# Kernel optimization log

Measured on AMD Instinct MI355X. Metric: run time of the kernel, lower is better.

The kernel has to match this reference:

```python
import jax, jax.numpy as jnp
import numpy as np

EMBED_DIM = 1024
NUM_HEADS = 16
HEAD_DIM = EMBED_DIM // NUM_HEADS
FF_HIDDEN = 4096
ROPE_BASE = 10000.0


def rope(x, start_pos):
    # x: [B, H, S, hd]; interleaved pair rotation
    S, hd = x.shape[2], x.shape[3]
    freqs = 1.0 / ROPE_BASE ** (jnp.arange(0, hd, 2, dtype=jnp.float32) / hd)
    t = jnp.arange(start_pos, start_pos + S, dtype=jnp.float32)
    angles = jnp.outer(t, freqs)            # [S, hd/2]
    cos, sin = jnp.cos(angles), jnp.sin(angles)
    x_even = x[..., 0::2]
    x_odd = x[..., 1::2]
    out_even = x_even * cos - x_odd * sin
    out_odd = x_even * sin + x_odd * cos
    return jnp.stack((out_even, out_odd), axis=-1).reshape(x.shape)


def rmsnorm(x, w, eps=1e-6):
    rms = jnp.sqrt(jnp.mean(x * x, axis=-1, keepdims=True) + eps)
    return x / rms * w


def setup_inputs() -> dict:
    key = jax.random.key(0)
    ks = jax.random.split(key, 8)
    D, H = EMBED_DIM, FF_HIDDEN
    s = lambda fin: 1.0 / np.sqrt(fin)
    return {
        "x": jax.random.normal(ks[0], (2, 2048, D), dtype=jnp.float32),
        "start_pos": 0,
        "norm1_w": jnp.ones((D,), jnp.float32),
        "w_qkv": jax.random.uniform(ks[1], (3 * D, D), jnp.float32, -s(D), s(D)),
        "w_o": jax.random.uniform(ks[2], (D, D), jnp.float32, -s(D), s(D)),
        "norm2_w": jnp.ones((D,), jnp.float32),
        "w_gate": jax.random.uniform(ks[3], (H, D), jnp.float32, -s(D), s(D)),
        "w_up": jax.random.uniform(ks[4], (H, D), jnp.float32, -s(D), s(D)),
        "w_down": jax.random.uniform(ks[5], (D, H), jnp.float32, -s(H), s(H)),
    }


def attention(x, w_qkv, w_o, start_pos):
    B, S, D = x.shape
    qkv = x @ w_qkv.T                         # [B, S, 3D]
    q, k, v = jnp.split(qkv, 3, axis=-1)
    def heads(t):
        return t.reshape(B, S, NUM_HEADS, HEAD_DIM).transpose(0, 2, 1, 3)
    q, k, v = heads(q), heads(k), heads(v)    # [B, H, S, hd]
    q = rope(q, start_pos)
    k = rope(k, start_pos)
    scores = jnp.einsum('bhqd,bhkd->bhqk', q, k) / np.sqrt(HEAD_DIM)
    causal = jnp.tril(jnp.ones((S, S), dtype=bool))
    scores = jnp.where(causal, scores, -jnp.inf)
    attn = jax.nn.softmax(scores, axis=-1)
    out = jnp.einsum('bhqk,bhkd->bhqd', attn, v)
    out = out.transpose(0, 2, 1, 3).reshape(B, S, D)
    return out @ w_o.T


def ffn(x, w_gate, w_up, w_down):
    return (jax.nn.silu(x @ w_gate.T) * (x @ w_up.T)) @ w_down.T


def reference(x, start_pos, norm1_w, w_qkv, w_o, norm2_w, w_gate, w_up, w_down):
    x = x + attention(rmsnorm(x, norm1_w), w_qkv, w_o, start_pos)
    x = x + ffn(rmsnorm(x, norm2_w), w_gate, w_up, w_down)
    return x
```

## Files before the change

### kernel.cpp

```cpp
#include <hip/hip_runtime.h>
#include <math.h>

typedef __bf16 bf16_t;
typedef __bf16 bf16x2 __attribute__((ext_vector_type(2)));
typedef __bf16 bf16x4 __attribute__((ext_vector_type(4)));
typedef __bf16 bf16x8 __attribute__((ext_vector_type(8)));
typedef float f32x4 __attribute__((ext_vector_type(4)));

#define B_ 2
#define S_ 2048
#define D_ 1024
#define NH 16
#define HD 64
#define FF 4096
#define NTOK (B_*S_)

__device__ __forceinline__ f32x4 mfma16(bf16x8 a, bf16x8 b, f32x4 c) {
  return __builtin_amdgcn_mfma_f32_16x16x32_bf16(a, b, c, 0, 0, 0);
}

__device__ __forceinline__ void gld_lds16(const bf16_t* g, bf16_t* l) {
  __builtin_amdgcn_global_load_lds(
      (const __attribute__((address_space(1))) void*)g,
      (__attribute__((address_space(3))) void*)l, 16, 0, 0);
}

__global__ __launch_bounds__(256) void cvt5_kernel(
    const float* __restrict__ p0, const float* __restrict__ p1,
    const float* __restrict__ p2, const float* __restrict__ p3,
    const float* __restrict__ p4,
    bf16_t* __restrict__ o0, bf16_t* __restrict__ o1, bf16_t* __restrict__ o2,
    bf16_t* __restrict__ o3, bf16_t* __restrict__ o4) {
  int i = blockIdx.x * 256 + threadIdx.x;
  const int stride = gridDim.x * 256;
  const int n = 4194304;
  for (; i < n; i += stride) {
    const float* src; bf16_t* dst; int j = i;
    if (j < 786432) { src = p0; dst = o0; }
    else {
      j -= 786432;
      if (j < 262144) { src = p1; dst = o1; }
      else {
        j -= 262144;
        if (j < 1048576) { src = p2; dst = o2; }
        else {
          j -= 1048576;
          if (j < 1048576) { src = p3; dst = o3; }
          else { j -= 1048576; src = p4; dst = o4; }
        }
      }
    }
    float4 v = ((const float4*)src)[j];
    bf16x4 ov;
    ov[0] = (bf16_t)v.x; ov[1] = (bf16_t)v.y; ov[2] = (bf16_t)v.z; ov[3] = (bf16_t)v.w;
    ((bf16x4*)dst)[j] = ov;
  }
}

__global__ __launch_bounds__(256) void rmsnorm_kernel(const float* __restrict__ x,
                                                      const float* __restrict__ w,
                                                      bf16_t* __restrict__ o) {
  const int row = blockIdx.x;
  const float4 v = ((const float4*)(x + (size_t)row * D_))[threadIdx.x];
  float s = v.x*v.x + v.y*v.y + v.z*v.z + v.w*v.w;
  #pragma unroll
  for (int d = 32; d; d >>= 1) s += __shfl_down(s, d);
  __shared__ float acc[4];
  if ((threadIdx.x & 63) == 0) acc[threadIdx.x >> 6] = s;
  __syncthreads();
  const float scale = rsqrtf((acc[0] + acc[1] + acc[2] + acc[3]) * (1.f / D_) + 1e-6f);
  const float4 wv = ((const float4*)w)[threadIdx.x];
  bf16x4 ov;
  ov[0] = (bf16_t)(v.x * scale * wv.x);
  ov[1] = (bf16_t)(v.y * scale * wv.y);
  ov[2] = (bf16_t)(v.z * scale * wv.z);
  ov[3] = (bf16_t)(v.w * scale * wv.w);
  ((bf16x4*)(o + (size_t)row * D_))[threadIdx.x] = ov;
}

template<int MODE, int BN>
__global__ __launch_bounds__(256) void gemm_kernel(
    const bf16_t* __restrict__ A, const bf16_t* __restrict__ W,
    int M, int N, int K,
    float* __restrict__ outF, bf16_t* __restrict__ outB,
    const float* __restrict__ res, const bf16_t* __restrict__ gate) {
  constexpr int NB = BN / 32;
  __shared__ __align__(16) bf16_t lA[2][128 * 32];
  __shared__ __align__(16) bf16_t lB[2][BN * 32];
  const int tid = threadIdx.x;
  const int wave = tid >> 6, lane = tid & 63;
  const int r = lane & 15, kg = lane >> 4;
  const int bm = blockIdx.y * 128, bn = blockIdx.x * BN;
  const int wr = (wave >> 1) * 64, wc = (wave & 1) * (BN / 2);
  const bf16_t* Ab = A + (size_t)bm * K;
  const bf16_t* Wb = W + (size_t)bn * K;

  auto stage = [&](int buf, int k0) {
    const int cb0 = (wave << 6);
    const int c0 = cb0 + lane;
    gld_lds16(Ab + (size_t)(c0 >> 2) * K + k0 + (c0 & 3) * 8, lA[buf] + cb0 * 8);
    const int cb1 = cb0 + 256;
    const int c1 = cb1 + lane;
    gld_lds16(Ab + (size_t)(c1 >> 2) * K + k0 + (c1 & 3) * 8, lA[buf] + cb1 * 8);
    gld_lds16(Wb + (size_t)(c0 >> 2) * K + k0 + (c0 & 3) * 8, lB[buf] + cb0 * 8);
    if (BN == 128)
      gld_lds16(Wb + (size_t)(c1 >> 2) * K + k0 + (c1 & 3) * 8, lB[buf] + cb1 * 8);
  };

  f32x4 acc[4][NB] = {};
  stage(0, 0);
  asm volatile("s_waitcnt vmcnt(0)" ::: "memory");
  __syncthreads();
  int cur = 0;
  for (int k0 = 0; k0 < K; k0 += 32) {
    if (k0 + 32 < K) stage(cur ^ 1, k0 + 32);
    const bf16_t* cA = lA[cur];
    const bf16_t* cB = lB[cur];
    bf16x8 af[4], bfr[NB];
    #pragma unroll
    for (int m = 0; m < 4; ++m)
      af[m] = *(const bf16x8*)&cA[(wr + m * 16 + r) * 32 + kg * 8];
    #pragma unroll
    for (int n = 0; n < NB; ++n)
      bfr[n] = *(const bf16x8*)&cB[(wc + n * 16 + r) * 32 + kg * 8];
    #pragma unroll
    for (int m = 0; m < 4; ++m)
      #pragma unroll
      for (int n = 0; n < NB; ++n)
        acc[m][n] = mfma16(af[m], bfr[n], acc[m][n]);
    asm volatile("s_waitcnt vmcnt(0)" ::: "memory");
    __syncthreads();
    cur ^= 1;
  }
  #pragma unroll
  for (int m = 0; m < 4; ++m) {
    const int row0 = bm + wr + m * 16 + kg * 4;
    #pragma unroll
    for (int n = 0; n < NB; ++n) {
      const int col = bn + wc + n * 16 + r;
      #pragma unroll
      for (int g2 = 0; g2 < 4; ++g2) {
        const size_t idx = (size_t)(row0 + g2) * N + col;
        const float v = acc[m][n][g2];
        if (MODE == 0) {
          outB[idx] = (bf16_t)v;
        } else if (MODE == 1) {
          outF[idx] = v + res[idx];
        } else {
          const float gf = (float)gate[idx];
          outB[idx] = (bf16_t)(v * gf / (1.f + __expf(-gf)));
        }
      }
    }
  }
}

__global__ __launch_bounds__(256) void rope_kernel(const bf16_t* __restrict__ qkv,
                                                   bf16_t* __restrict__ q_r,
                                                   bf16_t* __restrict__ k_r,
                                                   const int* __restrict__ start_pos) {
  const int bs = blockIdx.x;
  const int b = bs >> 11, s = bs & (S_ - 1);
  const float t = (float)(s + start_pos[0]);
  const bf16_t* rowp = qkv + (size_t)bs * 3072;
  #pragma unroll
  for (int i = 0; i < 4; ++i) {
    const int p = threadIdx.x + 256 * i;
    const int mat = p >> 9;
    const int rem = p & 511;
    const int h = rem >> 5, d2 = rem & 31;
    const float freq = exp2f((float)d2 * -0.4152410118609203f);
    float sn, cs;
    sincosf(t * freq, &sn, &cs);
    const float qs = mat ? 1.0f : 0.18033688011112042f;
    const bf16x2 e2 = *(const bf16x2*)(rowp + mat * 1024 + h * 64 + 2 * d2);
    const float e = (float)e2[0], od = (float)e2[1];
    bf16x2 ov;
    ov[0] = (bf16_t)((e * cs - od * sn) * qs);
    ov[1] = (bf16_t)((e * sn + od * cs) * qs);
    bf16_t* dst = (mat ? k_r : q_r) + ((size_t)(b * NH + h) * S_ + s) * HD + 2 * d2;
    *(bf16x2*)dst = ov;
  }
}

__global__ __launch_bounds__(256) void vtrans_kernel(const bf16_t* __restrict__ qkv,
                                                     bf16_t* __restrict__ vt) {
  const int bh = blockIdx.y, b = bh >> 4, h = bh & 15;
  const int s0 = blockIdx.x * 64;
  __shared__ bf16_t tile[64][65];
  #pragma unroll
  for (int i = 0; i < 16; ++i) {
    const int idx = threadIdx.x + 256 * i;
    const int sl = idx >> 6, d = idx & 63;
    tile[sl][d] = qkv[(size_t)(b * S_ + s0 + sl) * 3072 + 2048 + h * 64 + d];
  }
  __syncthreads();
  #pragma unroll
  for (int i = 0; i < 16; ++i) {
    const int idx = threadIdx.x + 256 * i;
    const int dl = idx >> 6, sl = idx & 63;
    vt[((size_t)bh * HD + dl) * S_ + s0 + sl] = tile[sl][dl];
  }
}

__global__ __launch_bounds__(256, 4) void attn_kernel(const bf16_t* __restrict__ qr,
                                                      const bf16_t* __restrict__ kr,
                                                      const bf16_t* __restrict__ vt,
                                                      bf16_t* __restrict__ out) {
  const int lid = blockIdx.x + 32 * blockIdx.y;
  const int xcd = lid & 7, slot = lid >> 3;
  const int bh = xcd * 4 + (slot >> 5);
  const int bx = slot & 31;
  const int b = bh >> 4, h = bh & 15;
  const int wave = threadIdx.x >> 6, lane = threadIdx.x & 63;
  const int pl = wave >> 1, sub = wave & 1;
  const int r = lane & 15, kg = lane >> 4;
  const int pairIdx = bx * 2 + pl;
  const bf16_t* kb_p = kr + (size_t)bh * S_ * HD;
  const bf16_t* vb_p = vt + (size_t)bh * HD * S_;

  __shared__ __align__(16) f32x4 lo[2][4][64];
  __shared__ float lm[2][64], ll[2][64];

  auto kv_block = [&](int kb, int qbase, const bf16x8& qf0, const bf16x8& qf1,
                      f32x4* o, float& m, float& l, bool masked) {
    f32x4 st[4];
    #pragma unroll
    for (int f = 0; f < 4; ++f) {
      const bf16_t* kp = kb_p + (size_t)(kb + f * 16 + r) * HD;
      f32x4 z = {};
      z = mfma16(*(const bf16x8*)&kp[kg * 8], qf0, z);
      z = mfma16(*(const bf16x8*)&kp[32 + kg * 8], qf1, z);
      st[f] = z;
    }
    float sc[4][4];
    float mx = -1e30f;
    #pragma unroll
    for (int f = 0; f < 4; ++f)
      #pragma unroll
      for (int g2 = 0; g2 < 4; ++g2) {
        float v = st[f][g2];
        if (masked) {
          const int k = kb + f * 16 + kg * 4 + g2;
          v = (k <= qbase + r) ? v : -1e30f;
        }
        sc[f][g2] = v;
        mx = fmaxf(mx, v);
      }
    mx = fmaxf(mx, __shfl_xor(mx, 16));
    mx = fmaxf(mx, __shfl_xor(mx, 32));
    float alpha = 1.f;
    const bool need = !__all(mx - m <= 8.f);
    if (need) {
      const float nm = fmaxf(m, mx);
      alpha = exp2f(m - nm);
      m = nm;
    }
    float psum = 0.f;
    float pe[4][4];
    #pragma unroll
    for (int f = 0; f < 4; ++f)
      #pragma unroll
      for (int g2 = 0; g2 < 4; ++g2) {
        const float p = exp2f(sc[f][g2] - m);
        pe[f][g2] = p;
        psum += p;
      }
    psum += __shfl_xor(psum, 16);
    psum += __shfl_xor(psum, 32);
    l = l * alpha + psum;
    bf16x8 PA[2];
    #pragma unroll
    for (int fa = 0; fa < 2; ++fa) {
      bf16x8 v;
      #pragma unroll
      for (int j = 0; j < 4; ++j) v[j] = (bf16_t)pe[2 * fa][j];
      #pragma unroll
      for (int j = 0; j < 4; ++j) v[4 + j] = (bf16_t)pe[2 * fa + 1][j];
      PA[fa] = v;
    }
    if (need) {
      float av[4];
      #pragma unroll
      for (int g2 = 0; g2 < 4; ++g2) av[g2] = __shfl(alpha, kg * 4 + g2);
      #pragma unroll
      for (int dblk = 0; dblk < 4; ++dblk)
        #pragma unroll
        for (int g2 = 0; g2 < 4; ++g2) o[dblk][g2] *= av[g2];
    }
    #pragma unroll
    for (int dblk = 0; dblk < 4; ++dblk) {
      const bf16_t* vp = vb_p + (size_t)(dblk * 16 + r) * S_ + kb;
      #pragma unroll
      for (int fa = 0; fa < 2; ++fa) {
        union { bf16x8 v; bf16x4 hf[2]; } bv;
        bv.hf[0] = *(const bf16x4*)&vp[fa * 32 + kg * 4];
        bv.hf[1] = *(const bf16x4*)&vp[fa * 32 + 16 + kg * 4];
        o[dblk] = mfma16(PA[fa], bv.v, o[dblk]);
      }
    }
  };

  auto run_chunk = [&](int qbase, f32x4* o, float& m, float& l) {
    const bf16_t* qp = qr + ((size_t)bh * S_ + qbase) * HD;
    const bf16x8 qf0 = *(const bf16x8*)&qp[r * HD + kg * 8];
    const bf16x8 qf1 = *(const bf16x8*)&qp[r * HD + 32 + kg * 8];
    int kb = sub * 64;
    for (; kb + 64 <= qbase; kb += 128)
      kv_block(kb, qbase, qf0, qf1, o, m, l, false);
    if (kb < qbase + 16)
      kv_block(kb, qbase, qf0, qf1, o, m, l, true);
  };

  auto write_partial = [&](const f32x4* o, float m, float l) {
    #pragma unroll
    for (int dblk = 0; dblk < 4; ++dblk) lo[pl][dblk][lane] = o[dblk];
    lm[pl][lane] = m;
    ll[pl][lane] = l;
  };

  auto finalize = [&](int qbase, const f32x4* o, float m, float l) {
    const float m1 = lm[pl][lane], l1 = ll[pl][lane];
    const float ms = fmaxf(m, m1);
    const float a0 = exp2f(m - ms), a1 = exp2f(m1 - ms);
    const float lt = l * a0 + l1 * a1;
    float av0[4], av1[4], lv[4];
    #pragma unroll
    for (int g2 = 0; g2 < 4; ++g2) {
      av0[g2] = __shfl(a0, kg * 4 + g2);
      av1[g2] = __shfl(a1, kg * 4 + g2);
      lv[g2]  = __shfl(lt, kg * 4 + g2);
    }
    #pragma unroll
    for (int dblk = 0; dblk < 4; ++dblk) {
      const f32x4 o1 = lo[pl][dblk][lane];
      #pragma unroll
      for (int g2 = 0; g2 < 4; ++g2) {
        const int srow = qbase + kg * 4 + g2;
        out[(size_t)(b * S_ + srow) * D_ + h * HD + dblk * 16 + r] =
            (bf16_t)((o[dblk][g2] * av0[g2] + o1[g2] * av1[g2]) / lv[g2]);
      }
    }
  };

  {
    const int qbase = pairIdx * 16;
    f32x4 o[4] = {};
    float m = -1e30f, l = 0.f;
    run_chunk(qbase, o, m, l);
    if (sub == 1) write_partial(o, m, l);
    __syncthreads();
    if (sub == 0) finalize(qbase, o, m, l);
  }
  {
    const int qbase = (127 - pairIdx) * 16;
    f32x4 o[4] = {};
    float m = -1e30f, l = 0.f;
    run_chunk(qbase, o, m, l);
    if (sub == 0) write_partial(o, m, l);
    __syncthreads();
    if (sub == 1) finalize(qbase, o, m, l);
  }
}

extern "C" void kernel_launch(void* const* d_in, const int* in_sizes, int n_in,
                              void* d_out, int out_size, void* d_ws, size_t ws_size,
                              hipStream_t stream) {
  const float* x     = (const float*)d_in[0];
  const int*   sp    = (const int*)d_in[1];
  const float* n1w   = (const float*)d_in[2];
  const float* wqkv  = (const float*)d_in[3];
  const float* wo    = (const float*)d_in[4];
  const float* n2w   = (const float*)d_in[5];
  const float* wgate = (const float*)d_in[6];
  const float* wup   = (const float*)d_in[7];
  const float* wdown = (const float*)d_in[8];

  char* p = (char*)d_ws;
  bf16_t* wqkv_b = (bf16_t*)p; p += (size_t)3 * D_ * D_ * 2;
  bf16_t* wo_b   = (bf16_t*)p; p += (size_t)D_ * D_ * 2;
  bf16_t* wg_b   = (bf16_t*)p; p += (size_t)FF * D_ * 2;
  bf16_t* wu_b   = (bf16_t*)p; p += (size_t)FF * D_ * 2;
  bf16_t* wd_b   = (bf16_t*)p; p += (size_t)FF * D_ * 2;
  bf16_t* xn     = (bf16_t*)p; p += (size_t)NTOK * D_ * 2;
  float*  x1     = (float*)p;  p += (size_t)NTOK * D_ * 4;
  char* pool = p;
  bf16_t* qkv    = (bf16_t*)(pool);
  bf16_t* q_r    = (bf16_t*)(pool + (size_t)25165824);
  bf16_t* k_r    = (bf16_t*)(pool + (size_t)33554432);
  bf16_t* v_t    = (bf16_t*)(pool + (size_t)41943040);
  bf16_t* attn_o = (bf16_t*)(pool + (size_t)50331648);
  bf16_t* gbuf   = (bf16_t*)(pool);
  bf16_t* hbuf   = (bf16_t*)(pool + (size_t)33554432);

  cvt5_kernel<<<dim3(2048), dim3(256), 0, stream>>>(
      wqkv, wo, wgate, wup, wdown, wqkv_b, wo_b, wg_b, wu_b, wd_b);

  rmsnorm_kernel<<<dim3(NTOK), dim3(256), 0, stream>>>(x, n1w, xn);

  gemm_kernel<0,128><<<dim3(3 * D_ / 128, NTOK / 128), dim3(256), 0, stream>>>(
      xn, wqkv_b, NTOK, 3 * D_, D_, nullptr, qkv, nullptr, nullptr);

  rope_kernel<<<dim3(NTOK), dim3(256), 0, stream>>>(qkv, q_r, k_r, sp);
  vtrans_kernel<<<dim3(S_ / 64, B_ * NH), dim3(256), 0, stream>>>(qkv, v_t);

  attn_kernel<<<dim3(32, B_ * NH), dim3(256), 0, stream>>>(q_r, k_r, v_t, attn_o);

  gemm_kernel<1,64><<<dim3(D_ / 64, NTOK / 128), dim3(256), 0, stream>>>(
      attn_o, wo_b, NTOK, D_, D_, x1, nullptr, x, nullptr);

  rmsnorm_kernel<<<dim3(NTOK), dim3(256), 0, stream>>>(x1, n2w, xn);

  gemm_kernel<0,128><<<dim3(FF / 128, NTOK / 128), dim3(256), 0, stream>>>(
      xn, wg_b, NTOK, FF, D_, nullptr, gbuf, nullptr, nullptr);

  gemm_kernel<2,128><<<dim3(FF / 128, NTOK / 128), dim3(256), 0, stream>>>(
      xn, wu_b, NTOK, FF, D_, nullptr, hbuf, nullptr, gbuf);

  gemm_kernel<1,64><<<dim3(D_ / 64, NTOK / 128), dim3(256), 0, stream>>>(
      hbuf, wd_b, NTOK, D_, FF, (float*)d_out, nullptr, x1, nullptr);
}
```

Baseline: 556.3 us.

## Split attention KV range across four waves and swizzle GEMM blocks per XCD

The attention kernel now assigns one query-chunk pair per block, with all four waves splitting the KV range (stride 256) instead of two waves per chunk. Partial softmax states are merged through shared memory, with each wave writing one 16-column slice of the output. The grid doubles, and the launch bound now asks for 8 blocks per CU, which limits registers per thread. The GEMM kernel also remaps block IDs so that consecutive tiles land on the same XCD, aiming for better L2 reuse, at the cost of an extra barrier and more LDS traffic in the merge.

```diff
diff --git a/kernel.cpp b/kernel.cpp
--- a/kernel.cpp
+++ b/kernel.cpp
@@ -90,7 +90,12 @@
   const int tid = threadIdx.x;
   const int wave = tid >> 6, lane = tid & 63;
   const int r = lane & 15, kg = lane >> 4;
-  const int bm = blockIdx.y * 128, bn = blockIdx.x * BN;
+  const int nx = gridDim.x;
+  const int nwg = nx * gridDim.y;
+  const int orig = blockIdx.y * nx + blockIdx.x;
+  const int q8 = nwg >> 3;
+  const int wgid = (orig & 7) * q8 + (orig >> 3);
+  const int bm = (wgid / nx) * 128, bn = (wgid % nx) * BN;
   const int wr = (wave >> 1) * 64, wc = (wave & 1) * (BN / 2);
   const bf16_t* Ab = A + (size_t)bm * K;
   const bf16_t* Wb = W + (size_t)bn * K;
@@ -203,24 +208,22 @@
   }
 }
 
-__global__ __launch_bounds__(256, 4) void attn_kernel(const bf16_t* __restrict__ qr,
+__global__ __launch_bounds__(256, 8) void attn_kernel(const bf16_t* __restrict__ qr,
                                                       const bf16_t* __restrict__ kr,
                                                       const bf16_t* __restrict__ vt,
                                                       bf16_t* __restrict__ out) {
-  const int lid = blockIdx.x + 32 * blockIdx.y;
+  const int lid = blockIdx.y * 64 + blockIdx.x;
   const int xcd = lid & 7, slot = lid >> 3;
-  const int bh = xcd * 4 + (slot >> 5);
-  const int bx = slot & 31;
+  const int bh = xcd * 4 + (slot >> 6);
+  const int pairIdx = slot & 63;
   const int b = bh >> 4, h = bh & 15;
   const int wave = threadIdx.x >> 6, lane = threadIdx.x & 63;
-  const int pl = wave >> 1, sub = wave & 1;
   const int r = lane & 15, kg = lane >> 4;
-  const int pairIdx = bx * 2 + pl;
   const bf16_t* kb_p = kr + (size_t)bh * S_ * HD;
   const bf16_t* vb_p = vt + (size_t)bh * HD * S_;
 
-  __shared__ __align__(16) f32x4 lo[2][4][64];
-  __shared__ float lm[2][64], ll[2][64];
+  __shared__ __align__(16) f32x4 lo[4][4][64];
+  __shared__ float lm[4][64], ll[4][64];
 
   auto kv_block = [&](int kb, int qbase, const bf16x8& qf0, const bf16x8& qf1,
                       f32x4* o, float& m, float& l, bool masked) {
@@ -305,41 +308,47 @@
     const bf16_t* qp = qr + ((size_t)bh * S_ + qbase) * HD;
     const bf16x8 qf0 = *(const bf16x8*)&qp[r * HD + kg * 8];
     const bf16x8 qf1 = *(const bf16x8*)&qp[r * HD + 32 + kg * 8];
-    int kb = sub * 64;
-    for (; kb + 64 <= qbase; kb += 128)
+    int kb = wave * 64;
+    for (; kb + 64 <= qbase; kb += 256)
       kv_block(kb, qbase, qf0, qf1, o, m, l, false);
     if (kb < qbase + 16)
       kv_block(kb, qbase, qf0, qf1, o, m, l, true);
   };
 
-  auto write_partial = [&](const f32x4* o, float m, float l) {
-    #pragma unroll
-    for (int dblk = 0; dblk < 4; ++dblk) lo[pl][dblk][lane] = o[dblk];
-    lm[pl][lane] = m;
-    ll[pl][lane] = l;
+  auto store_partial = [&](const f32x4* o, float m, float l) {
+    #pragma unroll
+    for (int d = 0; d < 4; ++d) lo[wave][d][lane] = o[d];
+    lm[wave][lane] = m;
+    ll[wave][lane] = l;
   };
 
-  auto finalize = [&](int qbase, const f32x4* o, float m, float l) {
-    const float m1 = lm[pl][lane], l1 = ll[pl][lane];
-    const float ms = fmaxf(m, m1);
-    const float a0 = exp2f(m - ms), a1 = exp2f(m1 - ms);
-    const float lt = l * a0 + l1 * a1;
-    float av0[4], av1[4], lv[4];
+  auto merge_write = [&](int qbase) {
+    const float ms = fmaxf(fmaxf(lm[0][lane], lm[1][lane]),
+                           fmaxf(lm[2][lane], lm[3][lane]));
+    float a[4], lt = 0.f;
+    #pragma unroll
+    for (int i = 0; i < 4; ++i) {
+      a[i] = exp2f(lm[i][lane] - ms);
+      lt += ll[i][lane] * a[i];
+    }
+    f32x4 oc = {};
+    #pragma unroll
+    for (int i = 0; i < 4; ++i) {
+      const f32x4 oi = lo[i][wave][lane];
+      float av[4];
+      #pragma unroll
+      for (int g2 = 0; g2 < 4; ++g2) av[g2] = __shfl(a[i], kg * 4 + g2);
+      #pragma unroll
+      for (int g2 = 0; g2 < 4; ++g2) oc[g2] += oi[g2] * av[g2];
+    }
+    float lv[4];
+    #pragma unroll
+    for (int g2 = 0; g2 < 4; ++g2) lv[g2] = __shfl(lt, kg * 4 + g2);
     #pragma unroll
     for (int g2 = 0; g2 < 4; ++g2) {
-      av0[g2] = __shfl(a0, kg * 4 + g2);
-      av1[g2] = __shfl(a1, kg * 4 + g2);
-      lv[g2]  = __shfl(lt, kg * 4 + g2);
-    }
-    #pragma unroll
-    for (int dblk = 0; dblk < 4; ++dblk) {
-      const f32x4 o1 = lo[pl][dblk][lane];
-      #pragma unroll
-      for (int g2 = 0; g2 < 4; ++g2) {
-        const int srow = qbase + kg * 4 + g2;
-        out[(size_t)(b * S_ + srow) * D_ + h * HD + dblk * 16 + r] =
-            (bf16_t)((o[dblk][g2] * av0[g2] + o1[g2] * av1[g2]) / lv[g2]);
-      }
+      const int srow = qbase + kg * 4 + g2;
+      out[(size_t)(b * S_ + srow) * D_ + h * HD + wave * 16 + r] =
+          (bf16_t)(oc[g2] / lv[g2]);
     }
   };
 
@@ -348,18 +357,19 @@
     f32x4 o[4] = {};
     float m = -1e30f, l = 0.f;
     run_chunk(qbase, o, m, l);
-    if (sub == 1) write_partial(o, m, l);
+    store_partial(o, m, l);
     __syncthreads();
-    if (sub == 0) finalize(qbase, o, m, l);
+    merge_write(qbase);
+    __syncthreads();
   }
   {
     const int qbase = (127 - pairIdx) * 16;
     f32x4 o[4] = {};
     float m = -1e30f, l = 0.f;
     run_chunk(qbase, o, m, l);
-    if (sub == 0) write_partial(o, m, l);
+    store_partial(o, m, l);
     __syncthreads();
-    if (sub == 1) finalize(qbase, o, m, l);
+    merge_write(qbase);
   }
 }
 
@@ -404,7 +414,7 @@
   rope_kernel<<<dim3(NTOK), dim3(256), 0, stream>>>(qkv, q_r, k_r, sp);
   vtrans_kernel<<<dim3(S_ / 64, B_ * NH), dim3(256), 0, stream>>>(qkv, v_t);
 
-  attn_kernel<<<dim3(32, B_ * NH), dim3(256), 0, stream>>>(q_r, k_r, v_t, attn_o);
+  attn_kernel<<<dim3(64, B_ * NH), dim3(256), 0, stream>>>(q_r, k_r, v_t, attn_o);
 
   gemm_kernel<1,64><<<dim3(D_ / 64, NTOK / 128), dim3(256), 0, stream>>>(
       attn_o, wo_b, NTOK, D_, D_, x1, nullptr, x, nullptr);
```

Result: slower. 615.1 us (+10.6%).
